# Kernel tuning notes

Hardware: AMD Instinct MI355X
Metric: run time of the kernel (lower is better)

The kernel has to match this reference:

```python
import jax, jax.numpy as jnp
import numpy as np

IN_FEATURES = 4096
OUT_FEATURES = 4096
CODESZ = 8
CODEBOOK_SIZE = 256


def fwht(x):
    """Normalized fast Walsh-Hadamard transform over the last dim (power of 2).
    Equivalent to x @ (H / sqrt(n)); H symmetric so this serves both
    matmul_hadUt and matmul_hadU in the power-of-2 case (had=None, K=1)."""
    orig_shape = x.shape
    n = orig_shape[-1]
    x = x.reshape(-1, n)
    h = 2
    while h <= n:
        x = x.reshape(-1, n // h, 2, h // 2)
        a, b = x[..., 0, :], x[..., 1, :]
        x = jnp.stack([a + b, a - b], axis=-2)
        h *= 2
    x = x.reshape(orig_shape)
    return x * (1.0 / np.sqrt(n)).astype(np.float32)


def setup_inputs() -> dict:
    key = jax.random.key(0)
    k1, k2, k3, k4, k5, k6 = jax.random.split(key, 6)
    x = jax.random.normal(k1, (4, 2048, IN_FEATURES), dtype=jnp.float32)
    Qidxs = jax.random.randint(k2, (OUT_FEATURES, IN_FEATURES // CODESZ), 0, CODEBOOK_SIZE, dtype=jnp.int32)
    grid = jax.random.normal(k3, (CODEBOOK_SIZE, CODESZ), dtype=jnp.float32)
    SU = jax.random.uniform(k4, (IN_FEATURES,), dtype=jnp.float32)
    SV = jax.random.uniform(k5, (OUT_FEATURES,), dtype=jnp.float32)
    bias = jax.random.normal(k6, (OUT_FEATURES,), dtype=jnp.float32)
    return {"x": x, "Qidxs": Qidxs, "grid": grid, "SU": SU, "SV": SV, "bias": bias}


def reference(x, Qidxs, grid, SU, SV, bias):
    lead = x.shape[:-1]
    h = x.reshape(-1, IN_FEATURES)            # [T, in]
    h = h * SU                                 # scale by SU
    h = fwht(h)                                # matmul_hadUt (input rotation)
    # codebook dequant: gather code vectors and form W_hat [out, in]
    W_hat = grid[Qidxs].reshape(OUT_FEATURES, IN_FEATURES)
    y = h @ W_hat.T                            # [T, out]
    y = fwht(y)[:, :OUT_FEATURES]              # matmul_hadU (output rotation)
    y = y * SV
    y = y.reshape(*lead, OUT_FEATURES) + bias
    return y
```

## Files before the change

kernel.cpp:

```cpp
#include <hip/hip_runtime.h>

#define IN_F 4096
#define OUT_F 4096
#define NROWS 8192
#define BK 32
#define NT (IN_F / BK)

typedef __attribute__((ext_vector_type(4))) float f32x4;
typedef __attribute__((ext_vector_type(8))) short bf16x8;
typedef __attribute__((ext_vector_type(8))) unsigned short u16x8;

__device__ __forceinline__ unsigned short f2bf(float f) {
  union { float f; unsigned u; } x; x.f = f;
  unsigned r = x.u + 0x7FFFu + ((x.u >> 16) & 1u);
  return (unsigned short)(r >> 16);
}

__device__ __forceinline__ void gload_lds16(const unsigned short* g, unsigned short* l) {
  __builtin_amdgcn_global_load_lds((__attribute__((address_space(1))) void*)g,
                                   (__attribute__((address_space(3))) void*)l,
                                   16, 0, 0);
}

__device__ __forceinline__ void bfly16(float v[16]) {
#pragma unroll
  for (int s = 1; s < 16; s <<= 1) {
#pragma unroll
    for (int i = 0; i < 16; ++i) {
      if (!(i & s)) { float a = v[i], b = v[i + s]; v[i] = a + b; v[i + s] = a - b; }
    }
  }
}

__global__ __launch_bounds__(256) void dequant_kernel(const int* __restrict__ Q,
                                                      const float* __restrict__ grid,
                                                      unsigned short* __restrict__ Wb) {
  int g = blockIdx.x * 256 + threadIdx.x;
  int idx = Q[g];
  const f32x4* gp = (const f32x4*)(grid + idx * 8);
  f32x4 v0 = gp[0], v1 = gp[1];
  u16x8 o;
  o[0] = f2bf(v0[0]); o[1] = f2bf(v0[1]); o[2] = f2bf(v0[2]); o[3] = f2bf(v0[3]);
  o[4] = f2bf(v1[0]); o[5] = f2bf(v1[1]); o[6] = f2bf(v1[2]); o[7] = f2bf(v1[3]);
  *(u16x8*)(Wb + (size_t)g * 8) = o;
}

__global__ __launch_bounds__(256) void fwht1_kernel(const float* __restrict__ x,
                                                    const float* __restrict__ SU,
                                                    unsigned short* __restrict__ Hb) {
  __shared__ float buf[4096];
  int tid = threadIdx.x;
  size_t rbase = (size_t)blockIdx.x * IN_F;
  const f32x4* x4 = (const f32x4*)(x + rbase);
  const f32x4* su4 = (const f32x4*)SU;
  f32x4* b4 = (f32x4*)buf;
#pragma unroll
  for (int s = 0; s < 4; ++s) {
    int c = tid + 256 * s;
    f32x4 v = x4[c];
    f32x4 u = su4[c];
    v.x *= u.x; v.y *= u.y; v.z *= u.z; v.w *= u.w;
    b4[c] = v;
  }
  __syncthreads();
  float v[16];
  {
#pragma unroll
    for (int j = 0; j < 4; ++j) {
      f32x4 t4 = b4[tid * 4 + j];
      v[j*4+0] = t4.x; v[j*4+1] = t4.y; v[j*4+2] = t4.z; v[j*4+3] = t4.w;
    }
    bfly16(v);
#pragma unroll
    for (int j = 0; j < 4; ++j) {
      f32x4 t4; t4.x = v[j*4+0]; t4.y = v[j*4+1]; t4.z = v[j*4+2]; t4.w = v[j*4+3];
      b4[tid * 4 + j] = t4;
    }
  }
  __syncthreads();
  {
    int lo = tid & 15, hi = tid >> 4;
    int base = lo + (hi << 8);
#pragma unroll
    for (int j = 0; j < 16; ++j) v[j] = buf[base + (j << 4)];
    bfly16(v);
#pragma unroll
    for (int j = 0; j < 16; ++j) buf[base + (j << 4)] = v[j];
  }
  __syncthreads();
  {
#pragma unroll
    for (int j = 0; j < 16; ++j) v[j] = buf[tid + (j << 8)];
    bfly16(v);
#pragma unroll
    for (int j = 0; j < 16; ++j)
      Hb[rbase + tid + (j << 8)] = f2bf(v[j] * 0.015625f);
  }
}

#define MM(i, A, B) acc[i] = __builtin_amdgcn_mfma_f32_16x16x32_bf16(A, B, acc[i], 0, 0, 0)

__global__ __launch_bounds__(512) void gemm256_kernel(const unsigned short* __restrict__ Hb,
                                                      const unsigned short* __restrict__ Wb,
                                                      float* __restrict__ Y) {
  __shared__ unsigned short lds[4][2][256 * BK];
  const int tid = threadIdx.x;
  const int lane = tid & 63;
  const int wid = tid >> 6;
  const int wr = wid >> 2;
  const int wc = wid & 3;
  const int lrow = lane & 15;
  const int kgrp = lane >> 4;

  const int bid = blockIdx.x;
  const int swz = (bid & 7) * 64 + (bid >> 3);
  const int brow = (swz >> 4) << 8;
  const int bcol = (swz & 15) << 8;

  const unsigned short* Ab = Hb + (size_t)brow * IN_F;
  const unsigned short* Bb = Wb + (size_t)bcol * IN_F;

  const int r0 = tid >> 2;
  const int sc = ((tid & 3) ^ ((r0 >> 1) & 3)) << 3;
  const unsigned short* Ag0 = Ab + (size_t)r0 * IN_F + sc;
  const unsigned short* Ag1 = Ab + (size_t)(r0 + 128) * IN_F + sc;
  const unsigned short* Bg0 = Bb + (size_t)r0 * IN_F + sc;
  const unsigned short* Bg1 = Bb + (size_t)(r0 + 128) * IN_F + sc;

#define STAGE(t, s) { \
  gload_lds16(Ag0 + (t) * BK, &lds[s][0][tid * 8]); \
  gload_lds16(Ag1 + (t) * BK, &lds[s][0][(tid + 512) * 8]); \
  gload_lds16(Bg0 + (t) * BK, &lds[s][1][tid * 8]); \
  gload_lds16(Bg1 + (t) * BK, &lds[s][1][(tid + 512) * 8]); }

  auto fragLd = [&](const unsigned short* base, int R) -> bf16x8 {
    return *(const bf16x8*)(base + R * BK + ((kgrp ^ ((R >> 1) & 3)) << 3));
  };

  const int ar = wr * 128 + lrow;
  const int br = wc * 64 + lrow;

#define READ_SET(aS, bS, slot) { \
  const unsigned short* As_ = &lds[slot][0][0]; \
  const unsigned short* Bs_ = &lds[slot][1][0]; \
  aS[0] = fragLd(As_, ar +   0); aS[1] = fragLd(As_, ar +  16); \
  aS[2] = fragLd(As_, ar +  32); aS[3] = fragLd(As_, ar +  48); \
  aS[4] = fragLd(As_, ar +  64); aS[5] = fragLd(As_, ar +  80); \
  aS[6] = fragLd(As_, ar +  96); aS[7] = fragLd(As_, ar + 112); \
  bS[0] = fragLd(Bs_, br +   0); bS[1] = fragLd(Bs_, br +  16); \
  bS[2] = fragLd(Bs_, br +  32); bS[3] = fragLd(Bs_, br +  48); }

#define MFMA_SET(aS, bS) { \
  __builtin_amdgcn_s_setprio(1); \
  MM( 0, aS[0], bS[0]); MM( 1, aS[0], bS[1]); MM( 2, aS[0], bS[2]); MM( 3, aS[0], bS[3]); \
  MM( 4, aS[1], bS[0]); MM( 5, aS[1], bS[1]); MM( 6, aS[1], bS[2]); MM( 7, aS[1], bS[3]); \
  MM( 8, aS[2], bS[0]); MM( 9, aS[2], bS[1]); MM(10, aS[2], bS[2]); MM(11, aS[2], bS[3]); \
  MM(12, aS[3], bS[0]); MM(13, aS[3], bS[1]); MM(14, aS[3], bS[2]); MM(15, aS[3], bS[3]); \
  MM(16, aS[4], bS[0]); MM(17, aS[4], bS[1]); MM(18, aS[4], bS[2]); MM(19, aS[4], bS[3]); \
  MM(20, aS[5], bS[0]); MM(21, aS[5], bS[1]); MM(22, aS[5], bS[2]); MM(23, aS[5], bS[3]); \
  MM(24, aS[6], bS[0]); MM(25, aS[6], bS[1]); MM(26, aS[6], bS[2]); MM(27, aS[6], bS[3]); \
  MM(28, aS[7], bS[0]); MM(29, aS[7], bS[1]); MM(30, aS[7], bS[2]); MM(31, aS[7], bS[3]); \
  __builtin_amdgcn_s_setprio(0); }

  f32x4 acc[32] = {};
  bf16x8 aA[8], bA[4], aB[8], bB[4];

  STAGE(0, 0); STAGE(1, 1); STAGE(2, 2);
  asm volatile("s_waitcnt vmcnt(4)" ::: "memory");
  asm volatile("s_barrier" ::: "memory");
  READ_SET(aA, bA, 0);

  for (int t = 0; t < NT; t += 2) {
    if (t) {
      if (t + 2 < NT) { asm volatile("s_waitcnt vmcnt(4)" ::: "memory"); }
      else            { asm volatile("s_waitcnt vmcnt(0)" ::: "memory"); }
      asm volatile("s_barrier" ::: "memory");
    }
    if (t + 3 < NT) STAGE(t + 3, (t + 3) & 3);
    READ_SET(aB, bB, (t + 1) & 3);
    MFMA_SET(aA, bA);

    if (t + 2 < NT) {
      if (t + 4 < NT) { asm volatile("s_waitcnt vmcnt(4)" ::: "memory"); }
      else            { asm volatile("s_waitcnt vmcnt(0)" ::: "memory"); }
      asm volatile("s_barrier" ::: "memory");
      if (t + 4 < NT) STAGE(t + 4, (t + 4) & 3);
      READ_SET(aA, bA, (t + 2) & 3);
    }
    MFMA_SET(aB, bB);
  }

#pragma unroll
  for (int mf = 0; mf < 8; ++mf) {
    int grow = brow + wr * 128 + mf * 16 + kgrp * 4;
    float* yp = Y + (size_t)grow * OUT_F + bcol + wc * 64 + lrow;
#pragma unroll
    for (int r = 0; r < 4; ++r)
#pragma unroll
      for (int n = 0; n < 4; ++n)
        yp[(size_t)r * OUT_F + n * 16] = acc[mf * 4 + n][r];
  }
#undef STAGE
#undef READ_SET
#undef MFMA_SET
}

__global__ __launch_bounds__(256) void fwht2_kernel(float* __restrict__ Y,
                                                    const float* __restrict__ SV,
                                                    const float* __restrict__ bias) {
  __shared__ float buf[4096];
  int tid = threadIdx.x;
  size_t rbase = (size_t)blockIdx.x * OUT_F;
  f32x4* y4 = (f32x4*)(Y + rbase);
  f32x4* b4 = (f32x4*)buf;
#pragma unroll
  for (int s = 0; s < 4; ++s) {
    int c = tid + 256 * s;
    b4[c] = y4[c];
  }
  __syncthreads();
  float v[16];
  {
#pragma unroll
    for (int j = 0; j < 4; ++j) {
      f32x4 t4 = b4[tid * 4 + j];
      v[j*4+0] = t4.x; v[j*4+1] = t4.y; v[j*4+2] = t4.z; v[j*4+3] = t4.w;
    }
    bfly16(v);
#pragma unroll
    for (int j = 0; j < 4; ++j) {
      f32x4 t4; t4.x = v[j*4+0]; t4.y = v[j*4+1]; t4.z = v[j*4+2]; t4.w = v[j*4+3];
      b4[tid * 4 + j] = t4;
    }
  }
  __syncthreads();
  {
    int lo = tid & 15, hi = tid >> 4;
    int base = lo + (hi << 8);
#pragma unroll
    for (int j = 0; j < 16; ++j) v[j] = buf[base + (j << 4)];
    bfly16(v);
#pragma unroll
    for (int j = 0; j < 16; ++j) buf[base + (j << 4)] = v[j];
  }
  __syncthreads();
  {
#pragma unroll
    for (int j = 0; j < 16; ++j) v[j] = buf[tid + (j << 8)];
    bfly16(v);
#pragma unroll
    for (int j = 0; j < 16; ++j) {
      int col = tid + (j << 8);
      Y[rbase + col] = v[j] * 0.015625f * SV[col] + bias[col];
    }
  }
}

extern "C" void kernel_launch(void* const* d_in, const int* in_sizes, int n_in,
                              void* d_out, int out_size, void* d_ws, size_t ws_size,
                              hipStream_t stream) {
  const float* x     = (const float*)d_in[0];
  const int*   Qidxs = (const int*)d_in[1];
  const float* grid  = (const float*)d_in[2];
  const float* SU    = (const float*)d_in[3];
  const float* SV    = (const float*)d_in[4];
  const float* bias  = (const float*)d_in[5];
  float* out = (float*)d_out;

  unsigned short* Wb = (unsigned short*)d_ws;
  unsigned short* Hb = Wb + (size_t)OUT_F * IN_F;

  hipLaunchKernelGGL(dequant_kernel, dim3((OUT_F * (IN_F / 8)) / 256), dim3(256), 0, stream,
                     Qidxs, grid, Wb);
  hipLaunchKernelGGL(fwht1_kernel, dim3(NROWS), dim3(256), 0, stream, x, SU, Hb);
  hipLaunchKernelGGL(gemm256_kernel, dim3((NROWS / 256) * (OUT_F / 256)), dim3(512), 0, stream,
                     Hb, Wb, out);
  hipLaunchKernelGGL(fwht2_kernel, dim3(NROWS), dim3(256), 0, stream, out, SV, bias);
}
```

Baseline: 357.6 us.

## Use 4-wave 256x256 GEMM blocks with 128x128 per-wave tiles and interleaved reads

The GEMM block shrinks from 8 to 4 waves, and each wave now computes a 128x128 output tile (64 accumulators) instead of 128x64. Each fragment loaded from LDS therefore feeds more MFMAs. The next tile's A and B fragment reads are now interleaved between groups of MFMAs, with sched_barriers and wait counts placed explicitly. The cost is much higher register pressure (256 accumulator VGPRs plus fragments) and fewer waves to hide latency, so spills or lower occupancy are possible.

```diff
diff --git a/kernel.cpp b/kernel.cpp
--- a/kernel.cpp
+++ b/kernel.cpp
@@ -98,17 +98,16 @@
   }
 }
 
-#define MM(i, A, B) acc[i] = __builtin_amdgcn_mfma_f32_16x16x32_bf16(A, B, acc[i], 0, 0, 0)
-
-__global__ __launch_bounds__(512) void gemm256_kernel(const unsigned short* __restrict__ Hb,
+
+__global__ __launch_bounds__(256) void gemm256_kernel(const unsigned short* __restrict__ Hb,
                                                       const unsigned short* __restrict__ Wb,
                                                       float* __restrict__ Y) {
   __shared__ unsigned short lds[4][2][256 * BK];
   const int tid = threadIdx.x;
   const int lane = tid & 63;
   const int wid = tid >> 6;
-  const int wr = wid >> 2;
-  const int wc = wid & 3;
+  const int wr = wid >> 1;
+  const int wc = wid & 1;
   const int lrow = lane & 15;
   const int kgrp = lane >> 4;
 
@@ -122,87 +121,101 @@
 
   const int r0 = tid >> 2;
   const int sc = ((tid & 3) ^ ((r0 >> 1) & 3)) << 3;
-  const unsigned short* Ag0 = Ab + (size_t)r0 * IN_F + sc;
-  const unsigned short* Ag1 = Ab + (size_t)(r0 + 128) * IN_F + sc;
-  const unsigned short* Bg0 = Bb + (size_t)r0 * IN_F + sc;
-  const unsigned short* Bg1 = Bb + (size_t)(r0 + 128) * IN_F + sc;
+  const unsigned short* Ag0 = Ab + (size_t)(r0 +   0) * IN_F + sc;
+  const unsigned short* Ag1 = Ab + (size_t)(r0 +  64) * IN_F + sc;
+  const unsigned short* Ag2 = Ab + (size_t)(r0 + 128) * IN_F + sc;
+  const unsigned short* Ag3 = Ab + (size_t)(r0 + 192) * IN_F + sc;
+  const unsigned short* Bg0 = Bb + (size_t)(r0 +   0) * IN_F + sc;
+  const unsigned short* Bg1 = Bb + (size_t)(r0 +  64) * IN_F + sc;
+  const unsigned short* Bg2 = Bb + (size_t)(r0 + 128) * IN_F + sc;
+  const unsigned short* Bg3 = Bb + (size_t)(r0 + 192) * IN_F + sc;
 
 #define STAGE(t, s) { \
   gload_lds16(Ag0 + (t) * BK, &lds[s][0][tid * 8]); \
-  gload_lds16(Ag1 + (t) * BK, &lds[s][0][(tid + 512) * 8]); \
+  gload_lds16(Ag1 + (t) * BK, &lds[s][0][(tid + 256) * 8]); \
+  gload_lds16(Ag2 + (t) * BK, &lds[s][0][(tid + 512) * 8]); \
+  gload_lds16(Ag3 + (t) * BK, &lds[s][0][(tid + 768) * 8]); \
   gload_lds16(Bg0 + (t) * BK, &lds[s][1][tid * 8]); \
-  gload_lds16(Bg1 + (t) * BK, &lds[s][1][(tid + 512) * 8]); }
+  gload_lds16(Bg1 + (t) * BK, &lds[s][1][(tid + 256) * 8]); \
+  gload_lds16(Bg2 + (t) * BK, &lds[s][1][(tid + 512) * 8]); \
+  gload_lds16(Bg3 + (t) * BK, &lds[s][1][(tid + 768) * 8]); }
 
   auto fragLd = [&](const unsigned short* base, int R) -> bf16x8 {
     return *(const bf16x8*)(base + R * BK + ((kgrp ^ ((R >> 1) & 3)) << 3));
   };
 
   const int ar = wr * 128 + lrow;
-  const int br = wc * 64 + lrow;
-
-#define READ_SET(aS, bS, slot) { \
-  const unsigned short* As_ = &lds[slot][0][0]; \
-  const unsigned short* Bs_ = &lds[slot][1][0]; \
+  const int br = wc * 128 + lrow;
+
+#define READ_A(t, aS) { const unsigned short* As_ = &lds[(t) & 3][0][0]; \
   aS[0] = fragLd(As_, ar +   0); aS[1] = fragLd(As_, ar +  16); \
   aS[2] = fragLd(As_, ar +  32); aS[3] = fragLd(As_, ar +  48); \
   aS[4] = fragLd(As_, ar +  64); aS[5] = fragLd(As_, ar +  80); \
-  aS[6] = fragLd(As_, ar +  96); aS[7] = fragLd(As_, ar + 112); \
+  aS[6] = fragLd(As_, ar +  96); aS[7] = fragLd(As_, ar + 112); }
+#define READ_B(t, bS) { const unsigned short* Bs_ = &lds[(t) & 3][1][0]; \
   bS[0] = fragLd(Bs_, br +   0); bS[1] = fragLd(Bs_, br +  16); \
-  bS[2] = fragLd(Bs_, br +  32); bS[3] = fragLd(Bs_, br +  48); }
-
-#define MFMA_SET(aS, bS) { \
+  bS[2] = fragLd(Bs_, br +  32); bS[3] = fragLd(Bs_, br +  48); \
+  bS[4] = fragLd(Bs_, br +  64); bS[5] = fragLd(Bs_, br +  80); \
+  bS[6] = fragLd(Bs_, br +  96); bS[7] = fragLd(Bs_, br + 112); }
+
+#define MM(i, A, B) acc[i] = __builtin_amdgcn_mfma_f32_16x16x32_bf16(A, B, acc[i], 0, 0, 0)
+#define MMROW(mf, aS, bS) { \
+  MM((mf)*8+0, aS[mf], bS[0]); MM((mf)*8+1, aS[mf], bS[1]); \
+  MM((mf)*8+2, aS[mf], bS[2]); MM((mf)*8+3, aS[mf], bS[3]); \
+  MM((mf)*8+4, aS[mf], bS[4]); MM((mf)*8+5, aS[mf], bS[5]); \
+  MM((mf)*8+6, aS[mf], bS[6]); MM((mf)*8+7, aS[mf], bS[7]); }
+
+#define TILE_BODY(t, aC_, bC_, aN_, bN_) { \
+  if ((t) + 2 < NT) { asm volatile("s_waitcnt vmcnt(8)" ::: "memory"); } \
+  else              { asm volatile("s_waitcnt vmcnt(0)" ::: "memory"); } \
+  __builtin_amdgcn_s_barrier(); \
+  if ((t) + 3 < NT) STAGE((t) + 3, ((t) + 3) & 3); \
+  asm volatile("s_waitcnt lgkmcnt(0)" ::: "memory"); \
+  __builtin_amdgcn_sched_barrier(0); \
   __builtin_amdgcn_s_setprio(1); \
-  MM( 0, aS[0], bS[0]); MM( 1, aS[0], bS[1]); MM( 2, aS[0], bS[2]); MM( 3, aS[0], bS[3]); \
-  MM( 4, aS[1], bS[0]); MM( 5, aS[1], bS[1]); MM( 6, aS[1], bS[2]); MM( 7, aS[1], bS[3]); \
-  MM( 8, aS[2], bS[0]); MM( 9, aS[2], bS[1]); MM(10, aS[2], bS[2]); MM(11, aS[2], bS[3]); \
-  MM(12, aS[3], bS[0]); MM(13, aS[3], bS[1]); MM(14, aS[3], bS[2]); MM(15, aS[3], bS[3]); \
-  MM(16, aS[4], bS[0]); MM(17, aS[4], bS[1]); MM(18, aS[4], bS[2]); MM(19, aS[4], bS[3]); \
-  MM(20, aS[5], bS[0]); MM(21, aS[5], bS[1]); MM(22, aS[5], bS[2]); MM(23, aS[5], bS[3]); \
-  MM(24, aS[6], bS[0]); MM(25, aS[6], bS[1]); MM(26, aS[6], bS[2]); MM(27, aS[6], bS[3]); \
-  MM(28, aS[7], bS[0]); MM(29, aS[7], bS[1]); MM(30, aS[7], bS[2]); MM(31, aS[7], bS[3]); \
+  MMROW(0, aC_, bC_); MMROW(1, aC_, bC_); \
+  __builtin_amdgcn_s_setprio(0); \
+  if ((t) + 1 < NT) READ_A((t) + 1, aN_); \
+  __builtin_amdgcn_sched_barrier(0); \
+  __builtin_amdgcn_s_setprio(1); \
+  MMROW(2, aC_, bC_); MMROW(3, aC_, bC_); \
+  __builtin_amdgcn_s_setprio(0); \
+  if ((t) + 1 < NT) READ_B((t) + 1, bN_); \
+  __builtin_amdgcn_sched_barrier(0); \
+  __builtin_amdgcn_s_setprio(1); \
+  MMROW(4, aC_, bC_); MMROW(5, aC_, bC_); \
+  MMROW(6, aC_, bC_); MMROW(7, aC_, bC_); \
   __builtin_amdgcn_s_setprio(0); }
 
-  f32x4 acc[32] = {};
-  bf16x8 aA[8], bA[4], aB[8], bB[4];
+  f32x4 acc[64] = {};
+  bf16x8 aC[8], bC[8], aN[8], bN[8];
 
   STAGE(0, 0); STAGE(1, 1); STAGE(2, 2);
-  asm volatile("s_waitcnt vmcnt(4)" ::: "memory");
-  asm volatile("s_barrier" ::: "memory");
-  READ_SET(aA, bA, 0);
+  asm volatile("s_waitcnt vmcnt(16)" ::: "memory");
+  __builtin_amdgcn_s_barrier();
+  READ_A(0, aC); READ_B(0, bC);
 
   for (int t = 0; t < NT; t += 2) {
-    if (t) {
-      if (t + 2 < NT) { asm volatile("s_waitcnt vmcnt(4)" ::: "memory"); }
-      else            { asm volatile("s_waitcnt vmcnt(0)" ::: "memory"); }
-      asm volatile("s_barrier" ::: "memory");
-    }
-    if (t + 3 < NT) STAGE(t + 3, (t + 3) & 3);
-    READ_SET(aB, bB, (t + 1) & 3);
-    MFMA_SET(aA, bA);
-
-    if (t + 2 < NT) {
-      if (t + 4 < NT) { asm volatile("s_waitcnt vmcnt(4)" ::: "memory"); }
-      else            { asm volatile("s_waitcnt vmcnt(0)" ::: "memory"); }
-      asm volatile("s_barrier" ::: "memory");
-      if (t + 4 < NT) STAGE(t + 4, (t + 4) & 3);
-      READ_SET(aA, bA, (t + 2) & 3);
-    }
-    MFMA_SET(aB, bB);
+    TILE_BODY(t,     aC, bC, aN, bN);
+    TILE_BODY(t + 1, aN, bN, aC, bC);
   }
 
 #pragma unroll
   for (int mf = 0; mf < 8; ++mf) {
     int grow = brow + wr * 128 + mf * 16 + kgrp * 4;
-    float* yp = Y + (size_t)grow * OUT_F + bcol + wc * 64 + lrow;
+    float* yp = Y + (size_t)grow * OUT_F + bcol + wc * 128 + lrow;
 #pragma unroll
     for (int r = 0; r < 4; ++r)
 #pragma unroll
-      for (int n = 0; n < 4; ++n)
-        yp[(size_t)r * OUT_F + n * 16] = acc[mf * 4 + n][r];
+      for (int nf = 0; nf < 8; ++nf)
+        yp[(size_t)r * OUT_F + nf * 16] = acc[mf * 8 + nf][r];
   }
 #undef STAGE
-#undef READ_SET
-#undef MFMA_SET
+#undef READ_A
+#undef READ_B
+#undef MM
+#undef MMROW
+#undef TILE_BODY
 }
 
 __global__ __launch_bounds__(256) void fwht2_kernel(float* __restrict__ Y,
@@ -273,7 +286,7 @@
   hipLaunchKernelGGL(dequant_kernel, dim3((OUT_F * (IN_F / 8)) / 256), dim3(256), 0, stream,
                      Qidxs, grid, Wb);
   hipLaunchKernelGGL(fwht1_kernel, dim3(NROWS), dim3(256), 0, stream, x, SU, Hb);
-  hipLaunchKernelGGL(gemm256_kernel, dim3((NROWS / 256) * (OUT_F / 256)), dim3(512), 0, stream,
+  hipLaunchKernelGGL(gemm256_kernel, dim3((NROWS / 256) * (OUT_F / 256)), dim3(256), 0, stream,
                      Hb, Wb, out);
   hipLaunchKernelGGL(fwht2_kernel, dim3(NROWS), dim3(256), 0, stream, out, SV, bias);
 }
```

Result: slower. 771.8 us (+115.8%).
